# Performance work log

Hardware: AMD Instinct MI355X
Metric: run time of the kernel (lower is better)

The kernel has to match this reference:

```python
import jax, jax.numpy as jnp
import numpy as np

CTX, SP, HIST, NC = 168, 24, 336, 128
LAGS = [24, 48, 72, 96, 120, 144, 168, 0]  # lags_seq + [0]
NSEG = CTX // SP  # 7


def gru_cell(x, h, Wih, Whh, bih, bhh):
    # torch.nn.GRUCell math; x: (N, D), h: (N, H)
    gi = x @ Wih.T + bih
    gh = h @ Whh.T + bhh
    ir, iz, inn = jnp.split(gi, 3, axis=-1)
    hr, hz, hn = jnp.split(gh, 3, axis=-1)
    r = jax.nn.sigmoid(ir + hr)
    z = jax.nn.sigmoid(iz + hz)
    n = jnp.tanh(inn + r * hn)
    return (1.0 - z) * n + z * h


def lstm(x, h, c, Wih, Whh, b):
    # single-layer batch_first LSTM; x: (B, T, D); torch gate order i,f,g,o
    xw = jnp.einsum('btd,gd->btg', x, Wih) + b  # precompute input projection
    def step(carry, xt):
        h, c = carry
        gates = xt + h @ Whh.T
        i, f, g, o = jnp.split(gates, 4, axis=-1)
        c = jax.nn.sigmoid(f) * c + jax.nn.sigmoid(i) * jnp.tanh(g)
        h = jax.nn.sigmoid(o) * jnp.tanh(c)
        return (h, c), h
    (h, c), ys = jax.lax.scan(step, (h, c), jnp.swapaxes(xw, 0, 1))
    return jnp.swapaxes(ys, 0, 1), h, c


def setup_inputs() -> dict:
    key = jax.random.key(0)
    ks = jax.random.split(key, 20)
    B = 8192
    p = lambda k, shape: jax.random.normal(k, shape, jnp.float32) * 0.05
    return dict(
        feat_static_cat=jax.random.randint(ks[0], (B, 1), 0, 50),
        feat_static_real=jax.random.normal(ks[1], (B, 1), jnp.float32),
        past_time_feat=jax.random.normal(ks[2], (B, HIST, 4), jnp.float32),
        past_target=jax.random.uniform(ks[3], (B, HIST), jnp.float32),
        past_observed_values=jnp.ones((B, HIST), jnp.float32),
        future_time_feat=jax.random.normal(ks[4], (B, SP, 4), jnp.float32),
        emb_table=p(ks[5], (50, 16)),
        gru_Wih=p(ks[6], (3 * NC, 30)),
        gru_Whh=p(ks[7], (3 * NC, NC)),
        gru_bih=p(ks[8], (3 * NC,)),
        gru_bhh=p(ks[9], (3 * NC,)),
        enc_Wih=p(ks[10], (NSEG, 4 * NC, NC)),
        enc_Whh=p(ks[11], (NSEG, 4 * NC, NC)),
        enc_b=p(ks[12], (NSEG, 4 * NC)),
        dec_Wih=p(ks[13], (4 * NC, 180)),
        dec_Whh=p(ks[14], (4 * NC, NC)),
        dec_b=p(ks[15], (4 * NC,)),
        out_W=p(ks[16], (1, NC)),
        out_b=p(ks[17], (1,)),
    )


def reference(feat_static_cat, feat_static_real, past_time_feat, past_target,
              past_observed_values, future_time_feat,
              emb_table, gru_Wih, gru_Whh, gru_bih, gru_bhh,
              enc_Wih, enc_Whh, enc_b, dec_Wih, dec_Whh, dec_b,
              out_W, out_b):
    B = past_target.shape[0]
    time_feat = past_time_feat[:, HIST - CTX:, :]  # (B, CTX, 4)

    # lagged subsequences: lagged[:, j, k] = seq[:, HIST - lag_k - CTX + j]
    lags = jnp.stack(
        [past_target[:, HIST - lag - CTX: HIST - lag] for lag in LAGS], axis=-1
    )  # (B, CTX, 8)

    # MeanScaler over past_target[:, CTX:] (keepdim)
    data = past_target[:, CTX:]
    w = past_observed_values[:, CTX:]
    total_w = w.sum(axis=1)                     # (B,)
    wsum = (jnp.abs(data) * w).sum(axis=1)      # (B,)
    default_scale = wsum.sum() / jnp.maximum(total_w.sum(), 1.0)
    scale = wsum / jnp.maximum(total_w, 1.0)
    scale = jnp.maximum(1e-10, jnp.where(wsum > 0, scale, default_scale))
    scale = scale[:, None]                      # (B, 1)

    embedded = emb_table[feat_static_cat[:, 0]]  # (B, 16)
    static_feat = jnp.concatenate([embedded, feat_static_real, jnp.log(scale)], axis=1)  # (B, 18)
    rep_static = jnp.broadcast_to(static_feat[:, None, :], (B, CTX, static_feat.shape[-1]))

    lags_scaled = lags / scale[:, :, None]
    inputs = jnp.concatenate([lags_scaled, time_feat, rep_static], axis=-1)  # (B, CTX, 30)
    inputs = inputs.reshape(B, NSEG, SP, inputs.shape[-1])  # (B, 7, 24, 30)

    encoder_out = jnp.zeros((B, SP, NC), inputs.dtype)
    h = jnp.zeros((B, NC), inputs.dtype)
    c = jnp.zeros((B, NC), inputs.dtype)
    for i in range(NSEG):  # fixed small loop; each segment has distinct LSTM weights
        x = inputs[:, i].reshape(-1, inputs.shape[-1])  # (B*SP, 30)
        hv = gru_cell(x, encoder_out.reshape(-1, NC), gru_Wih, gru_Whh, gru_bih, gru_bhh)
        hv = hv.reshape(B, SP, NC)
        encoder_out, h, c = lstm(hv, h, c, enc_Wih[i], enc_Whh[i], enc_b[i])

    query = jnp.concatenate(
        [inputs[:, 0], encoder_out, future_time_feat, rep_static[:, -SP:, :]], axis=-1
    )  # (B, 24, 180)
    dec_out, _, _ = lstm(query, h, c, dec_Wih, dec_Whh, dec_b)
    outputs = dec_out @ out_W.T + out_b  # (B, 24, 1)
    return outputs * scale[:, :, None]
```

## Files before the change

### kernel.cpp

```cpp
#include <hip/hip_runtime.h>
#include <math.h>

typedef short bf16x8 __attribute__((ext_vector_type(8)));
typedef float f32x4 __attribute__((ext_vector_type(4)));
typedef unsigned short u16;
typedef unsigned int u32;

#define WSUMS 0
#define TOTWS 1
#define WSUM_OFF 2
#define TOTW_OFF 8194
#define SCL_F 16386
#define WB_BYTE 98432

#define GWI_U 0
#define GWH_U 12288
#define EO_U  61440
#define DO_U  978944
#define XG_U  1142784
#define XD_U  23162880

__constant__ int cLAG[8] = {144,120,96,72,48,24,0,168};

__device__ __forceinline__ float sig_(float x){ return __builtin_amdgcn_rcpf(1.0f+__expf(-x)); }
__device__ __forceinline__ float th_(float x){ float e=__expf(2.0f*x); return __builtin_fmaf(-2.0f, __builtin_amdgcn_rcpf(e+1.0f), 1.0f); }
__device__ __forceinline__ u16 f2b(float x){ u32 u=__float_as_uint(x); return (u16)((u + 0x7fffu + ((u>>16)&1u))>>16); }
__device__ __forceinline__ float b2f(u16 v){ return __uint_as_float(((u32)v)<<16); }
__device__ __forceinline__ u32 f2b_pk(float lo, float hi){
  u32 r; asm("v_cvt_pk_bf16_f32 %0, %1, %2" : "=v"(r) : "v"(lo), "v"(hi)); return r;
}
__device__ __forceinline__ void pin(bf16x8 &x){
  f32x4 t = __builtin_bit_cast(f32x4, x);
  asm volatile("" : "+v"(t));
  x = __builtin_bit_cast(bf16x8, t);
}

#define MFMA(a,b,c) __builtin_amdgcn_mfma_f32_16x16x32_bf16(a,b,c,0,0,0)

__global__ void scale_kernel(const float* __restrict__ tgt,
                             const float* __restrict__ obs,
                             float* __restrict__ ws)
{
  __shared__ float s1[256], s2[256];
  int b = blockIdx.x*256 + threadIdx.x;
  float wsum=0.f, totw=0.f;
  const float* tr = tgt + b*336 + 168;
  const float* wr = obs + b*336 + 168;
  for(int t=0;t<168;t++){ float w=wr[t]; wsum += fabsf(tr[t])*w; totw += w; }
  ws[WSUM_OFF + b] = wsum;
  ws[TOTW_OFF + b] = totw;
  s1[threadIdx.x]=wsum; s2[threadIdx.x]=totw;
  __syncthreads();
  for(int s=128;s>0;s>>=1){
    if(threadIdx.x<s){ s1[threadIdx.x]+=s1[threadIdx.x+s]; s2[threadIdx.x]+=s2[threadIdx.x+s]; }
    __syncthreads();
  }
  if(threadIdx.x==0){ atomicAdd(&ws[WSUMS], s1[0]); atomicAdd(&ws[TOTWS], s2[0]); }
}

__global__ void prep_w(const float* __restrict__ gWih, const float* __restrict__ gWhh,
                       const float* __restrict__ eWih, const float* __restrict__ eWhh,
                       const float* __restrict__ dWih, const float* __restrict__ dWhh,
                       float* __restrict__ ws)
{
  u16* WU = (u16*)((char*)ws + WB_BYTE);
  int tid = blockIdx.x*blockDim.x + threadIdx.x;
  int nt = gridDim.x*blockDim.x;
  for(int i=tid;i<12288;i+=nt){ int n=i>>5,k=i&31; WU[GWI_U+i]=(k<30)?f2b(gWih[n*30+k]):(u16)0; }
  for(int i=tid;i<49152;i+=nt){ int n=i>>7,k=i&127; WU[GWH_U+i]=f2b(gWhh[n*128+k]); }
  for(int i=tid;i<917504;i+=nt){
    int s=i>>17,r2=i&131071,n=r2>>8,k=r2&255;
    float v=(k<128)?eWih[(s*512+n)*128+k]:eWhh[(s*512+n)*128+(k-128)];
    WU[EO_U+i]=f2b(v);
  }
  for(int i=tid;i<163840;i+=nt){
    int n=i/320, k=i-n*320; float v;
    if(k<128)       v=dWih[n*180+30+k];
    else if(k<136)  v=dWih[n*180+(k-128)];
    else if(k<140)  v=dWih[n*180+8+(k-136)];
    else if(k<144)  v=dWih[n*180+158+(k-140)];
    else if(k<162)  v=dWih[n*180+12+(k-144)];
    else if(k<180)  v=dWih[n*180+162+(k-162)];
    else if(k<192)  v=0.f;
    else            v=dWhh[n*128+(k-192)];
    WU[DO_U+i]=f2b(v);
  }
}

__global__ void prep_x(const float* __restrict__ tgt, const float* __restrict__ ptf,
                       const float* __restrict__ ftf, float* __restrict__ ws)
{
  __shared__ float inv_l[64];
  u16* WU = (u16*)((char*)ws + WB_BYTE);
  const int tid = threadIdx.x;
  const int b0 = blockIdx.x*64;
  if(tid<64){
    int b=b0+tid;
    float wsumv=ws[WSUM_OFF+b], totw=ws[TOTW_OFF+b];
    float def=ws[WSUMS]/fmaxf(ws[TOTWS],1.f);
    float sc=fmaxf(1e-10f,(wsumv>0.f)?wsumv/fmaxf(totw,1.f):def);
    ws[SCL_F+b]=sc; inv_l[tid]=1.f/sc;
  }
  __syncthreads();
  for(int idx=tid; idx<64*168; idx+=256){
    int bl=idx/168, gt=idx-bl*168; int b=b0+bl;
    float iv=inv_l[bl];
    __align__(16) u16 row[16];
    #pragma unroll
    for(int j=0;j<8;j++) row[j]=f2b(tgt[b*336+cLAG[j]+gt]*iv);
    const float* pp=ptf+((size_t)(b*336+168+gt))*4;
    #pragma unroll
    for(int j=0;j<4;j++) row[8+j]=f2b(pp[j]);
    row[12]=row[13]=row[14]=row[15]=0;
    int seg=gt/24, t=gt-seg*24;
    u16* dst=WU+XG_U+(((size_t)seg*8192+b)*24+t)*16;
    *(uint4*)dst=*(const uint4*)row; *(uint4*)(dst+8)=*(const uint4*)(row+8);
  }
  for(int idx=tid; idx<64*24; idx+=256){
    int bl=idx/24, t=idx-bl*24; int b=b0+bl;
    float iv=inv_l[bl];
    __align__(16) u16 row[16];
    #pragma unroll
    for(int j=0;j<8;j++) row[j]=f2b(tgt[b*336+cLAG[j]+t]*iv);
    #pragma unroll
    for(int j=0;j<4;j++) row[8+j]=f2b(ptf[((size_t)(b*336+168+t))*4+j]);
    #pragma unroll
    for(int j=0;j<4;j++) row[12+j]=f2b(ftf[b*96+t*4+j]);
    u16* dst=WU+XD_U+((size_t)b*24+t)*16;
    *(uint4*)dst=*(const uint4*)row; *(uint4*)(dst+8)=*(const uint4*)(row+8);
  }
}

__global__ __launch_bounds__(512,2)
__attribute__((amdgpu_waves_per_eu(2,2)))
void deepar_main(const int* __restrict__ cat, const float* __restrict__ sreal,
                 const float* __restrict__ emb,
                 const float* __restrict__ gbih, const float* __restrict__ gbhh,
                 const float* __restrict__ encb, const float* __restrict__ decb,
                 const float* __restrict__ outW, const float* __restrict__ outb,
                 float* __restrict__ ws, float* __restrict__ out)
{
  asm volatile("" ::: "v252","v253","v254","v255");

  const u16* __restrict__ WU=(const u16*)((const char*)ws+WB_BYTE);

  __shared__ __align__(16) u16 encbuf[384*136];
  __shared__ __align__(16) u16 Ast[2][16*136];
  __shared__ __align__(16) u16 Xast[2][64*40];
  __shared__ __align__(16) u16 Xdast[16*72];
  __shared__ __align__(16) u16 hstash[2][16*136];
  __shared__ u16 statb[16][18];
  __shared__ float scl_s[16];
  __shared__ float outw_s[128];
  __shared__ float red[16][8];
  __shared__ float outb_s;

  const int tid=threadIdx.x;
  const int b0=blockIdx.x*16;
  const int wv=tid>>6, lane=tid&63, quad=lane>>4, l15=lane&15;

  if(tid<16) scl_s[tid]=ws[SCL_F+b0+tid];
  if(tid<128) outw_s[tid]=outW[tid];
  if(tid==128) outb_s=outb[0];
  if(tid>=256){ int q=tid-256; int r=q>>4,k=q&15; statb[r][k]=f2b(emb[cat[b0+r]*16+k]); }
  { const uint4 z4={0,0,0,0};
    for(int i=tid;i<6528;i+=512) *(uint4*)(encbuf+i*8)=z4;
    for(int i=tid;i<544;i+=512)  *(uint4*)(&hstash[0][0]+i*8)=z4;
  }
  __syncthreads();
  if(tid<16){ statb[tid][16]=f2b(sreal[b0+tid]); statb[tid][17]=f2b(logf(scl_s[tid])); }
  __syncthreads();
  for(int i=tid;i<1280;i+=512){ int a=i/20, k=i-a*20+12;
    u16 v=(k<30)?statb[a>>2][k-12]:(u16)0;
    Xast[0][a*40+k]=v; Xast[1][a*40+k]=v; }
  for(int i=tid;i<896;i+=512){ int rr=i/56, k=i-rr*56+16;
    u16 v; if(k<34) v=statb[rr][k-16]; else if(k<52) v=statb[rr][k-34]; else v=0;
    Xdast[rr*72+k]=v; }
  __syncthreads();

  float gbi[3], gbh[3];
  #pragma unroll
  for(int j=0;j<3;j++){ int nb=(wv+j*8)*16+l15; gbi[j]=gbih[nb]; gbh[j]=gbhh[nb]; }
  const float gb01[2] = { gbi[0]+gbh[0], gbi[1]+gbh[1] };

  float cst[4]={0.f,0.f,0.f,0.f};
  const int hc=wv*16+l15;
  int p=0;

  for(int seg=0;seg<7;seg++){
    bf16x8 gwi[3]; bf16x8 gwh[3][4];
    #pragma unroll
    for(int j=0;j<3;j++){
      int nb=(wv+j*8)*16+l15;
      gwi[j]=*(const bf16x8*)(WU+GWI_U+nb*32+quad*8); pin(gwi[j]);
      #pragma unroll
      for(int kt=0;kt<4;kt++){ gwh[j][kt]=*(const bf16x8*)(WU+GWH_U+nb*128+kt*32+quad*8); pin(gwh[j][kt]); }
    }

    for(int c=0;c<6;c++){
      u16* Xb = &Xast[c&1][0];
      if(tid<128){ int a=tid>>1;
        const u16* src=WU+XG_U+(((size_t)seg*8192+b0+(a>>2))*24+4*c+(a&3))*16;
        if(tid&1) *(uint2*)(Xb+a*40+8)=*(const uint2*)(src+8);
        else      *(uint4*)(Xb+a*40)  =*(const uint4*)src; }
      __syncthreads();

      f32x4 g01[2][4], a2[4], h2[4];
      #pragma unroll
      for(int mt=0;mt<4;mt++){
        g01[0][mt]=(f32x4){gb01[0],gb01[0],gb01[0],gb01[0]};
        g01[1][mt]=(f32x4){gb01[1],gb01[1],gb01[1],gb01[1]};
        a2[mt]   =(f32x4){gbi[2],gbi[2],gbi[2],gbi[2]};
        h2[mt]   =(f32x4){gbh[2],gbh[2],gbh[2],gbh[2]};
      }
      #pragma unroll
      for(int mt=0;mt<4;mt++){
        bf16x8 af=*(const bf16x8*)(Xb+(mt*16+l15)*40+quad*8);
        g01[0][mt]=MFMA(af,gwi[0],g01[0][mt]);
        g01[1][mt]=MFMA(af,gwi[1],g01[1][mt]);
        a2[mt]   =MFMA(af,gwi[2],a2[mt]);
      }
      const u16* ebase=encbuf+(size_t)(c*64)*136;
      #pragma unroll
      for(int kt=0;kt<4;kt++)
        #pragma unroll
        for(int mt=0;mt<4;mt++){
          bf16x8 af=*(const bf16x8*)(ebase+(mt*16+l15)*136+kt*32+quad*8);
          g01[0][mt]=MFMA(af,gwh[0][kt],g01[0][mt]);
          g01[1][mt]=MFMA(af,gwh[1][kt],g01[1][mt]);
          h2[mt]   =MFMA(af,gwh[2][kt],h2[mt]);
        }
      u16 hv16[4][4];
      #pragma unroll
      for(int mt=0;mt<4;mt++){
        float hv[4];
        #pragma unroll
        for(int reg=0;reg<4;reg++){
          int a=mt*16+quad*4+reg;
          float rg=sig_(g01[0][mt][reg]);
          float zg=sig_(g01[1][mt][reg]);
          float hp=b2f(encbuf[(c*64+a)*136+hc]);
          float nn=th_(a2[mt][reg]+rg*h2[mt][reg]);
          hv[reg]=(1.f-zg)*nn+zg*hp;
        }
        u32 p01=f2b_pk(hv[0],hv[1]), p23=f2b_pk(hv[2],hv[3]);
        hv16[mt][0]=(u16)p01; hv16[mt][1]=(u16)(p01>>16);
        hv16[mt][2]=(u16)p23; hv16[mt][3]=(u16)(p23>>16);
      }
      __syncthreads();
      #pragma unroll
      for(int mt=0;mt<4;mt++)
        #pragma unroll
        for(int reg=0;reg<4;reg++)
          encbuf[(c*64+mt*16+quad*4+reg)*136+hc]=hv16[mt][reg];
    }

    bf16x8 we[4][8]; float be[4];
    #pragma unroll
    for(int j=0;j<4;j++){
      int nb=(wv+j*8)*16+l15;
      be[j]=encb[seg*512+nb];
      #pragma unroll
      for(int kt=0;kt<8;kt++){
        we[j][kt]=*(const bf16x8*)(WU+EO_U+(size_t)seg*131072+nb*256+kt*32+quad*8);
        pin(we[j][kt]);
      }
    }
    for(int t=0;t<24;t++){
      int tb=(t>>2)*64+(t&3);
      u16* Ab=&Ast[t&1][0];
      if(tid<256){ int row=tid>>4,q=tid&15;
        *(uint4*)(Ab+row*136+q*8)=*(const uint4*)(encbuf+(tb+row*4)*136+q*8); }
      __syncthreads();
      const u16* Hb=&hstash[p][0];
      f32x4 acc[4];
      #pragma unroll
      for(int j=0;j<4;j++) acc[j]=(f32x4){be[j],be[j],be[j],be[j]};
      #pragma unroll
      for(int kt=0;kt<8;kt++){
        bf16x8 af=(kt<4)? *(const bf16x8*)(Ab+l15*136+kt*32+quad*8)
                        : *(const bf16x8*)(Hb+l15*136+(kt-4)*32+quad*8);
        #pragma unroll
        for(int j=0;j<4;j++) acc[j]=MFMA(af,we[j][kt],acc[j]);
      }
      u16 hnew[4];
      { float hf[4];
        #pragma unroll
        for(int reg=0;reg<4;reg++){
          float ig=sig_(acc[0][reg]),fg=sig_(acc[1][reg]);
          float gg=th_(acc[2][reg]), og=sig_(acc[3][reg]);
          float c_=fg*cst[reg]+ig*gg; cst[reg]=c_;
          hf[reg]=og*th_(c_);
        }
        u32 p01=f2b_pk(hf[0],hf[1]), p23=f2b_pk(hf[2],hf[3]);
        hnew[0]=(u16)p01; hnew[1]=(u16)(p01>>16);
        hnew[2]=(u16)p23; hnew[3]=(u16)(p23>>16);
      }
      int pn=p^1;
      u16* Hw=&hstash[pn][0];
      #pragma unroll
      for(int reg=0;reg<4;reg++){
        int row=quad*4+reg;
        Hw[row*136+hc]=hnew[reg];
        encbuf[(tb+row*4)*136+hc]=hnew[reg];
      }
      p=pn;
    }
  }

  bf16x8 wd[4][10]; float bd[4];
  #pragma unroll
  for(int j=0;j<4;j++){
    int nb=(wv+j*8)*16+l15;
    bd[j]=decb[nb];
    #pragma unroll
    for(int kt=0;kt<10;kt++){
      wd[j][kt]=*(const bf16x8*)(WU+DO_U+nb*320+kt*32+quad*8);
      pin(wd[j][kt]);
    }
  }
  for(int t=0;t<24;t++){
    int tb=(t>>2)*64+(t&3);
    u16* Ab=&Ast[t&1][0];
    if(tid<256){ int row=tid>>4,q=tid&15;
      *(uint4*)(Ab+row*136+q*8)=*(const uint4*)(encbuf+(tb+row*4)*136+q*8); }
    else if(tid<288){ int q=tid-256; int rr=q>>1;
      const u16* src=WU+XD_U+((size_t)(b0+rr)*24+t)*16;
      if(q&1) *(uint4*)(Xdast+rr*72+8)=*(const uint4*)(src+8);
      else    *(uint4*)(Xdast+rr*72)  =*(const uint4*)src; }
    __syncthreads();
    const u16* Hb=&hstash[p][0];
    f32x4 acc[4];
    #pragma unroll
    for(int j=0;j<4;j++) acc[j]=(f32x4){bd[j],bd[j],bd[j],bd[j]};
    #pragma unroll
    for(int kt=0;kt<10;kt++){
      bf16x8 af=(kt<4)? *(const bf16x8*)(Ab+l15*136+kt*32+quad*8)
              :(kt<6)? *(const bf16x8*)(Xdast+l15*72+(kt-4)*32+quad*8)
                     : *(const bf16x8*)(Hb+l15*136+(kt-6)*32+quad*8);
      #pragma unroll
      for(int j=0;j<4;j++) acc[j]=MFMA(af,wd[j][kt],acc[j]);
    }
    u16 hnew[4];
    { float hf[4];
      #pragma unroll
      for(int reg=0;reg<4;reg++){
        float ig=sig_(acc[0][reg]),fg=sig_(acc[1][reg]);
        float gg=th_(acc[2][reg]), og=sig_(acc[3][reg]);
        float c_=fg*cst[reg]+ig*gg; cst[reg]=c_;
        hf[reg]=og*th_(c_);
      }
      u32 p01=f2b_pk(hf[0],hf[1]), p23=f2b_pk(hf[2],hf[3]);
      hnew[0]=(u16)p01; hnew[1]=(u16)(p01>>16);
      hnew[2]=(u16)p23; hnew[3]=(u16)(p23>>16);
    }
    int pn=p^1;
    #pragma unroll
    for(int reg=0;reg<4;reg++)
      hstash[pn][(quad*4+reg)*136+hc]=hnew[reg];
    __syncthreads();
    if(tid<128){ int row=tid>>3,g=tid&7; float s=0.f;
      #pragma unroll
      for(int i=0;i<16;i++) s+=b2f(hstash[pn][row*136+g*16+i])*outw_s[g*16+i];
      red[row][g]=s; }
    __syncthreads();
    if(tid<16){ float s=outb_s;
      #pragma unroll
      for(int g=0;g<8;g++) s+=red[tid][g];
      out[(b0+tid)*24+t]=s*scl_s[tid]; }
    p=pn;
  }
}

extern "C" void kernel_launch(void* const* d_in, const int* in_sizes, int n_in,
                              void* d_out, int out_size, void* d_ws, size_t ws_size,
                              hipStream_t stream)
{
  (void)in_sizes; (void)n_in; (void)out_size; (void)ws_size;
  const int*   cat  = (const int*)d_in[0];
  const float* sreal= (const float*)d_in[1];
  const float* ptf  = (const float*)d_in[2];
  const float* tgt  = (const float*)d_in[3];
  const float* obs  = (const float*)d_in[4];
  const float* ftf  = (const float*)d_in[5];
  const float* emb  = (const float*)d_in[6];
  const float* gWih = (const float*)d_in[7];
  const float* gWhh = (const float*)d_in[8];
  const float* gbih = (const float*)d_in[9];
  const float* gbhh = (const float*)d_in[10];
  const float* eWih = (const float*)d_in[11];
  const float* eWhh = (const float*)d_in[12];
  const float* encb = (const float*)d_in[13];
  const float* dWih = (const float*)d_in[14];
  const float* dWhh = (const float*)d_in[15];
  const float* decb = (const float*)d_in[16];
  const float* outW = (const float*)d_in[17];
  const float* outb = (const float*)d_in[18];
  float* ws  = (float*)d_ws;
  float* out = (float*)d_out;

  hipMemsetAsync(d_ws, 0, 2*sizeof(float), stream);
  scale_kernel<<<dim3(8192/256), dim3(256), 0, stream>>>(tgt, obs, ws);
  prep_w<<<dim3(512), dim3(256), 0, stream>>>(gWih,gWhh,eWih,eWhh,dWih,dWhh,ws);
  prep_x<<<dim3(128), dim3(256), 0, stream>>>(tgt, ptf, ftf, ws);
  deepar_main<<<dim3(512), dim3(512), 0, stream>>>(cat,sreal,emb,gbih,gbhh,encb,decb,
                                                   outW,outb,ws,out);
}
```

Before: 1.029 ms.

## Fold log2e scaling into weights, feed biases as MFMA accumulators, prefetch GRU inputs

Pre-scales the gate weights and biases by log2(e), or 2·log2(e) for the tanh gates, during weight preparation. Sigmoid and tanh can then use the raw exp2 instruction without a per-element multiply. Bias vectors are passed straight into the first MFMA as the accumulator instead of being initialised separately. GRU input staging becomes a one-step-ahead prefetch into the alternate buffer, which drops a per-chunk barrier. The bf16 rounding of the pre-scaled weights slightly changes numerics, and dropping the barrier depends on later synchronisation to stay race-free.

```diff
diff --git a/kernel.cpp b/kernel.cpp
--- a/kernel.cpp
+++ b/kernel.cpp
@@ -20,10 +20,20 @@
 #define XG_U  1142784
 #define XD_U  23162880
 
+#define L2E 1.4426950408889634f
+#define T2E 2.8853900817779268f
+
 __constant__ int cLAG[8] = {144,120,96,72,48,24,0,168};
 
-__device__ __forceinline__ float sig_(float x){ return __builtin_amdgcn_rcpf(1.0f+__expf(-x)); }
-__device__ __forceinline__ float th_(float x){ float e=__expf(2.0f*x); return __builtin_fmaf(-2.0f, __builtin_amdgcn_rcpf(e+1.0f), 1.0f); }
+__device__ __forceinline__ float sig2(float x){
+  return __builtin_amdgcn_rcpf(1.0f+__builtin_amdgcn_exp2f(-x));
+}
+__device__ __forceinline__ float th2(float x){
+  return __builtin_fmaf(-2.0f, __builtin_amdgcn_rcpf(__builtin_amdgcn_exp2f(x)+1.0f), 1.0f);
+}
+__device__ __forceinline__ float thc(float x){
+  return th2(x*T2E);
+}
 __device__ __forceinline__ u16 f2b(float x){ u32 u=__float_as_uint(x); return (u16)((u + 0x7fffu + ((u>>16)&1u))>>16); }
 __device__ __forceinline__ float b2f(u16 v){ return __uint_as_float(((u32)v)<<16); }
 __device__ __forceinline__ u32 f2b_pk(float lo, float hi){
@@ -66,15 +76,21 @@
   u16* WU = (u16*)((char*)ws + WB_BYTE);
   int tid = blockIdx.x*blockDim.x + threadIdx.x;
   int nt = gridDim.x*blockDim.x;
-  for(int i=tid;i<12288;i+=nt){ int n=i>>5,k=i&31; WU[GWI_U+i]=(k<30)?f2b(gWih[n*30+k]):(u16)0; }
-  for(int i=tid;i<49152;i+=nt){ int n=i>>7,k=i&127; WU[GWH_U+i]=f2b(gWhh[n*128+k]); }
+  for(int i=tid;i<12288;i+=nt){ int n=i>>5,k=i&31;
+    float s=((n>>7)==2)?T2E:L2E;
+    WU[GWI_U+i]=(k<30)?f2b(gWih[n*30+k]*s):(u16)0; }
+  for(int i=tid;i<49152;i+=nt){ int n=i>>7,k=i&127;
+    float s=((n>>7)==2)?T2E:L2E;
+    WU[GWH_U+i]=f2b(gWhh[n*128+k]*s); }
   for(int i=tid;i<917504;i+=nt){
     int s=i>>17,r2=i&131071,n=r2>>8,k=r2&255;
+    float sc=((n>>7)==2)?T2E:L2E;
     float v=(k<128)?eWih[(s*512+n)*128+k]:eWhh[(s*512+n)*128+(k-128)];
-    WU[EO_U+i]=f2b(v);
+    WU[EO_U+i]=f2b(v*sc);
   }
   for(int i=tid;i<163840;i+=nt){
     int n=i/320, k=i-n*320; float v;
+    float sc=((n>>7)==2)?T2E:L2E;
     if(k<128)       v=dWih[n*180+30+k];
     else if(k<136)  v=dWih[n*180+(k-128)];
     else if(k<140)  v=dWih[n*180+8+(k-136)];
@@ -83,7 +99,7 @@
     else if(k<180)  v=dWih[n*180+162+(k-162)];
     else if(k<192)  v=0.f;
     else            v=dWhh[n*128+(k-192)];
-    WU[DO_U+i]=f2b(v);
+    WU[DO_U+i]=f2b(v*sc);
   }
 }
 
@@ -159,6 +175,17 @@
   const int b0=blockIdx.x*16;
   const int wv=tid>>6, lane=tid&63, quad=lane>>4, l15=lane&15;
 
+  auto stageX = [&](int gc){
+    if(tid<128 && gc<42){
+      int sg=gc/6, cc=gc-sg*6;
+      int a=tid>>1;
+      u16* Xb=&Xast[gc&1][0];
+      const u16* src=WU+XG_U+(((size_t)sg*8192+b0+(a>>2))*24+4*cc+(a&3))*16;
+      if(tid&1) *(uint2*)(Xb+a*40+8)=*(const uint2*)(src+8);
+      else      *(uint4*)(Xb+a*40)  =*(const uint4*)src;
+    }
+  };
+
   if(tid<16) scl_s[tid]=ws[SCL_F+b0+tid];
   if(tid<128) outw_s[tid]=outW[tid];
   if(tid==128) outb_s=outb[0];
@@ -176,12 +203,19 @@
   for(int i=tid;i<896;i+=512){ int rr=i/56, k=i-rr*56+16;
     u16 v; if(k<34) v=statb[rr][k-16]; else if(k<52) v=statb[rr][k-34]; else v=0;
     Xdast[rr*72+k]=v; }
+  stageX(0);
   __syncthreads();
 
   float gbi[3], gbh[3];
   #pragma unroll
-  for(int j=0;j<3;j++){ int nb=(wv+j*8)*16+l15; gbi[j]=gbih[nb]; gbh[j]=gbhh[nb]; }
-  const float gb01[2] = { gbi[0]+gbh[0], gbi[1]+gbh[1] };
+  for(int j=0;j<3;j++){ int nb=(wv+j*8)*16+l15;
+    float s=(j==2)?T2E:L2E;
+    gbi[j]=gbih[nb]*s; gbh[j]=gbhh[nb]*s; }
+  const float gbr=gbi[0]+gbh[0], gbz=gbi[1]+gbh[1];
+  const f32x4 b4r ={gbr,gbr,gbr,gbr};
+  const f32x4 b4z ={gbz,gbz,gbz,gbz};
+  const f32x4 b4i2={gbi[2],gbi[2],gbi[2],gbi[2]};
+  const f32x4 b4h2={gbh[2],gbh[2],gbh[2],gbh[2]};
 
   float cst[4]={0.f,0.f,0.f,0.f};
   const int hc=wv*16+l15;
@@ -198,27 +232,16 @@
     }
 
     for(int c=0;c<6;c++){
-      u16* Xb = &Xast[c&1][0];
-      if(tid<128){ int a=tid>>1;
-        const u16* src=WU+XG_U+(((size_t)seg*8192+b0+(a>>2))*24+4*c+(a&3))*16;
-        if(tid&1) *(uint2*)(Xb+a*40+8)=*(const uint2*)(src+8);
-        else      *(uint4*)(Xb+a*40)  =*(const uint4*)src; }
-      __syncthreads();
+      stageX(seg*6+c+1);
+      const u16* Xb = &Xast[c&1][0];
 
       f32x4 g01[2][4], a2[4], h2[4];
-      #pragma unroll
-      for(int mt=0;mt<4;mt++){
-        g01[0][mt]=(f32x4){gb01[0],gb01[0],gb01[0],gb01[0]};
-        g01[1][mt]=(f32x4){gb01[1],gb01[1],gb01[1],gb01[1]};
-        a2[mt]   =(f32x4){gbi[2],gbi[2],gbi[2],gbi[2]};
-        h2[mt]   =(f32x4){gbh[2],gbh[2],gbh[2],gbh[2]};
-      }
       #pragma unroll
       for(int mt=0;mt<4;mt++){
         bf16x8 af=*(const bf16x8*)(Xb+(mt*16+l15)*40+quad*8);
-        g01[0][mt]=MFMA(af,gwi[0],g01[0][mt]);
-        g01[1][mt]=MFMA(af,gwi[1],g01[1][mt]);
-        a2[mt]   =MFMA(af,gwi[2],a2[mt]);
+        g01[0][mt]=MFMA(af,gwi[0],b4r);
+        g01[1][mt]=MFMA(af,gwi[1],b4z);
+        a2[mt]   =MFMA(af,gwi[2],b4i2);
       }
       const u16* ebase=encbuf+(size_t)(c*64)*136;
       #pragma unroll
@@ -228,7 +251,7 @@
           bf16x8 af=*(const bf16x8*)(ebase+(mt*16+l15)*136+kt*32+quad*8);
           g01[0][mt]=MFMA(af,gwh[0][kt],g01[0][mt]);
           g01[1][mt]=MFMA(af,gwh[1][kt],g01[1][mt]);
-          h2[mt]   =MFMA(af,gwh[2][kt],h2[mt]);
+          h2[mt]   =MFMA(af,gwh[2][kt],(kt==0)?b4h2:h2[mt]);
         }
       u16 hv16[4][4];
       #pragma unroll
@@ -237,11 +260,11 @@
         #pragma unroll
         for(int reg=0;reg<4;reg++){
           int a=mt*16+quad*4+reg;
-          float rg=sig_(g01[0][mt][reg]);
-          float zg=sig_(g01[1][mt][reg]);
+          float rg=sig2(g01[0][mt][reg]);
+          float zg=sig2(g01[1][mt][reg]);
           float hp=b2f(encbuf[(c*64+a)*136+hc]);
-          float nn=th_(a2[mt][reg]+rg*h2[mt][reg]);
-          hv[reg]=(1.f-zg)*nn+zg*hp;
+          float nn=th2(__builtin_fmaf(rg,h2[mt][reg],a2[mt][reg]));
+          hv[reg]=__builtin_fmaf(zg,hp-nn,nn);
         }
         u32 p01=f2b_pk(hv[0],hv[1]), p23=f2b_pk(hv[2],hv[3]);
         hv16[mt][0]=(u16)p01; hv16[mt][1]=(u16)(p01>>16);
@@ -255,11 +278,12 @@
           encbuf[(c*64+mt*16+quad*4+reg)*136+hc]=hv16[mt][reg];
     }
 
-    bf16x8 we[4][8]; float be[4];
+    bf16x8 we[4][8]; f32x4 b4e[4];
     #pragma unroll
     for(int j=0;j<4;j++){
       int nb=(wv+j*8)*16+l15;
-      be[j]=encb[seg*512+nb];
+      float b=encb[seg*512+nb]*((j==2)?T2E:L2E);
+      b4e[j]=(f32x4){b,b,b,b};
       #pragma unroll
       for(int kt=0;kt<8;kt++){
         we[j][kt]=*(const bf16x8*)(WU+EO_U+(size_t)seg*131072+nb*256+kt*32+quad*8);
@@ -275,22 +299,20 @@
       const u16* Hb=&hstash[p][0];
       f32x4 acc[4];
       #pragma unroll
-      for(int j=0;j<4;j++) acc[j]=(f32x4){be[j],be[j],be[j],be[j]};
-      #pragma unroll
       for(int kt=0;kt<8;kt++){
         bf16x8 af=(kt<4)? *(const bf16x8*)(Ab+l15*136+kt*32+quad*8)
                         : *(const bf16x8*)(Hb+l15*136+(kt-4)*32+quad*8);
         #pragma unroll
-        for(int j=0;j<4;j++) acc[j]=MFMA(af,we[j][kt],acc[j]);
+        for(int j=0;j<4;j++) acc[j]=MFMA(af,we[j][kt],(kt==0)?b4e[j]:acc[j]);
       }
       u16 hnew[4];
       { float hf[4];
         #pragma unroll
         for(int reg=0;reg<4;reg++){
-          float ig=sig_(acc[0][reg]),fg=sig_(acc[1][reg]);
-          float gg=th_(acc[2][reg]), og=sig_(acc[3][reg]);
-          float c_=fg*cst[reg]+ig*gg; cst[reg]=c_;
-          hf[reg]=og*th_(c_);
+          float ig=sig2(acc[0][reg]),fg=sig2(acc[1][reg]);
+          float gg=th2(acc[2][reg]), og=sig2(acc[3][reg]);
+          float c_=__builtin_fmaf(fg,cst[reg],ig*gg); cst[reg]=c_;
+          hf[reg]=og*thc(c_);
         }
         u32 p01=f2b_pk(hf[0],hf[1]), p23=f2b_pk(hf[2],hf[3]);
         hnew[0]=(u16)p01; hnew[1]=(u16)(p01>>16);
@@ -308,11 +330,12 @@
     }
   }
 
-  bf16x8 wd[4][10]; float bd[4];
+  bf16x8 wd[4][10]; f32x4 b4d[4];
   #pragma unroll
   for(int j=0;j<4;j++){
     int nb=(wv+j*8)*16+l15;
-    bd[j]=decb[nb];
+    float b=decb[nb]*((j==2)?T2E:L2E);
+    b4d[j]=(f32x4){b,b,b,b};
     #pragma unroll
     for(int kt=0;kt<10;kt++){
       wd[j][kt]=*(const bf16x8*)(WU+DO_U+nb*320+kt*32+quad*8);
@@ -332,23 +355,21 @@
     const u16* Hb=&hstash[p][0];
     f32x4 acc[4];
     #pragma unroll
-    for(int j=0;j<4;j++) acc[j]=(f32x4){bd[j],bd[j],bd[j],bd[j]};
-    #pragma unroll
     for(int kt=0;kt<10;kt++){
       bf16x8 af=(kt<4)? *(const bf16x8*)(Ab+l15*136+kt*32+quad*8)
               :(kt<6)? *(const bf16x8*)(Xdast+l15*72+(kt-4)*32+quad*8)
                      : *(const bf16x8*)(Hb+l15*136+(kt-6)*32+quad*8);
       #pragma unroll
-      for(int j=0;j<4;j++) acc[j]=MFMA(af,wd[j][kt],acc[j]);
+      for(int j=0;j<4;j++) acc[j]=MFMA(af,wd[j][kt],(kt==0)?b4d[j]:acc[j]);
     }
     u16 hnew[4];
     { float hf[4];
       #pragma unroll
       for(int reg=0;reg<4;reg++){
-        float ig=sig_(acc[0][reg]),fg=sig_(acc[1][reg]);
-        float gg=th_(acc[2][reg]), og=sig_(acc[3][reg]);
-        float c_=fg*cst[reg]+ig*gg; cst[reg]=c_;
-        hf[reg]=og*th_(c_);
+        float ig=sig2(acc[0][reg]),fg=sig2(acc[1][reg]);
+        float gg=th2(acc[2][reg]), og=sig2(acc[3][reg]);
+        float c_=__builtin_fmaf(fg,cst[reg],ig*gg); cst[reg]=c_;
+        hf[reg]=og*thc(c_);
       }
       u32 p01=f2b_pk(hf[0],hf[1]), p23=f2b_pk(hf[2],hf[3]);
       hnew[0]=(u16)p01; hnew[1]=(u16)(p01>>16);
```

Result: faster. 939.2 us (-8.7%).
